# Optimization experiments

Hardware: AMD Instinct MI355X
Metric: run time of the kernel (lower is better)

The kernel has to match this reference:

```python
import jax, jax.numpy as jnp
import numpy as np

B, CIN, COUT, HIN = 2, 64, 64, 96
ALPHA = 0.2       # LeakyReLU slope in GAT
K_RANK = 6        # dist.argsort(1).argsort(1) <= 6  -> 7 nearest neighbors incl. self
DN = ('NCHW', 'OIHW', 'NCHW')


def setup_inputs():
    key = jax.random.key(0)
    ks = jax.random.split(key, 10)
    sc = lambda k, shape, s: jax.random.normal(k, shape, jnp.float32) * s
    return {
        'x': jax.random.normal(ks[0], (B, CIN, HIN, HIN), jnp.float32),
        'conv_w': sc(ks[1], (COUT, CIN, 3, 3), 0.05),
        'conv_b': jnp.zeros((COUT,), jnp.float32),
        'W1': sc(ks[2], (COUT, COUT), 0.1),
        'a1': sc(ks[3], (2 * COUT,), 0.1),
        'W2': sc(ks[4], (COUT, COUT), 0.1),
        'a2': sc(ks[5], (2 * COUT,), 0.1),
        'Wout': sc(ks[6], (2 * COUT, COUT), 0.1),
        'aout': sc(ks[7], (2 * COUT,), 0.1),
        'tconv_w': sc(ks[8], (COUT, COUT, 3, 3), 0.05),  # torch ConvTranspose2d layout [in,out,kh,kw]
        'tconv_b': jnp.zeros((COUT,), jnp.float32),
    }


def _gat_layer(h, adj, W, a, concat):
    # h: [B,N,F_in], W: [F_in,F_out], a: [2*F_out]
    Wh = h @ W                                   # [B,N,F']
    Fo = W.shape[1]
    e = (Wh @ a[:Fo])[:, :, None] + (Wh @ a[Fo:])[:, None, :]   # [B,N,N]
    e = jax.nn.leaky_relu(e, ALPHA)
    e = jnp.where(adj > 0, e, -9e15)
    attn = jax.nn.softmax(e, axis=-1)
    out = jnp.einsum('bij,bjf->bif', attn, Wh)
    return jax.nn.elu(out) if concat else out


def reference(x, conv_w, conv_b, W1, a1, W2, a2, Wout, aout, tconv_w, tconv_b):
    # --- Pre_ProcessLayer_Graph: stride-2 conv, flatten, 7-NN dense adjacency ---
    y = jax.lax.conv_general_dilated(x, conv_w, (2, 2), ((1, 1), (1, 1)),
                                     dimension_numbers=DN) + conv_b[None, :, None, None]
    Bb, C, H, W_ = y.shape
    N = H * W_
    feat = y.reshape(Bb, C, N).transpose(0, 2, 1)          # [B,N,C]
    sq = jnp.sum(feat * feat, axis=-1)                     # [B,N]
    d2 = sq[:, :, None] + sq[:, None, :] - 2.0 * jnp.einsum('bic,bjc->bij', feat, feat)
    dist = jnp.sqrt(jnp.maximum(d2, 0.0))                  # euclidean cdist
    ranks = jnp.argsort(jnp.argsort(dist, axis=-1), axis=-1)
    adj = (ranks <= K_RANK).astype(feat.dtype)             # [B,N,N] binary, incl. self (rank 0)
    # --- GAT (pyGAT style): 2 concat heads + output attention layer, eval mode ---
    h1 = _gat_layer(feat, adj, W1, a1, True)
    h2 = _gat_layer(feat, adj, W2, a2, True)
    hcat = jnp.concatenate([h1, h2], axis=-1)              # [B,N,2C]
    g = jax.nn.elu(_gat_layer(hcat, adj, Wout, aout, False))  # [B,N,C]
    # --- reshape back + transpose conv (k=3, s=2, p=1, output_padding=1) ---
    g = g.transpose(0, 2, 1).reshape(Bb, C, H, W_)
    wt = jnp.flip(tconv_w, (2, 3)).transpose(1, 0, 2, 3)   # -> [out,in,kh,kw]
    out = jax.lax.conv_general_dilated(g, wt, (1, 1), ((1, 2), (1, 2)),
                                       lhs_dilation=(2, 2),
                                       dimension_numbers=DN) + tconv_b[None, :, None, None]
    return out
```

## Files before the change

kernel.cpp:

```cpp
#include <hip/hip_runtime.h>
#include <hip/hip_bf16.h>
#include <stdint.h>

using bf16 = __hip_bfloat16;
using u64 = unsigned long long;

constexpr int B_ = 2;
constexpr int N_ = 2304;

constexpr int OFF_WC2   = 0;
constexpr int OFF_WT2   = 36864;
constexpr int OFF_W1F   = 73728;
constexpr int OFF_W2F   = 77824;
constexpr int OFF_WOUTF = 81920;
constexpr int OFF_A1F   = 90112;
constexpr int OFF_A2F   = 90240;
constexpr int OFF_AOUTF = 90368;
constexpr int OFF_CBF   = 90496;
constexpr int OFF_TBF   = 90560;
constexpr int OFF_FLAG  = 90624;
constexpr int OFF_SQ    = 90688;
constexpr int OFF_S11   = 95296;
constexpr int OFF_S12   = 99904;
constexpr int OFF_S21   = 104512;
constexpr int OFF_S22   = 109120;
constexpr int OFF_S1O   = 113728;
constexpr int OFF_S2O   = 118336;
constexpr int OFF_KNN   = 122944;
constexpr int OFF_BUF0  = 159808;
constexpr int OFF_BUF1  = 454720;
constexpr int OFF_BUF2  = 749632;
constexpr int OFF_BUF3  = 1044544;
constexpr int OFF_PK    = 1339456;

__device__ __forceinline__ float bf2f_raw(unsigned short u) {
    return __uint_as_float(((unsigned int)u) << 16);
}

__device__ __forceinline__ unsigned int mono32(float f) {
    unsigned int u = __float_as_uint(f);
    return (u & 0x80000000u) ? ~u : (u | 0x80000000u);
}

__device__ __forceinline__ bool detect_f32(const void* conv_w) {
    const unsigned short* cw = (const unsigned short*)conv_w;
    float m = 0.f;
    #pragma unroll
    for (int u = 0; u < 64; ++u) {
        float v = fabsf(bf2f_raw(cw[u]));
        if (v < 3.0e38f) m = fmaxf(m, v);
    }
    return m > 1.0e4f;
}

__global__ __launch_bounds__(256) void kc_prep(
    const void* conv_w, const void* conv_b, const void* W1, const void* a1,
    const void* W2, const void* a2, const void* Wout, const void* aout,
    const void* tconv_w, const void* tconv_b, float* __restrict__ ws)
{
    bool f32 = detect_f32(conv_w);
    int idx = blockIdx.x * 256 + threadIdx.x;
    if (idx == 0) ws[OFF_FLAG] = f32 ? 1.f : 0.f;
    if (idx < 32256) ws[OFF_SQ + idx] = 0.f;

    {
        int tap = idx >> 12, ic = (idx >> 6) & 63, oc = idx & 63;
        if (f32) {
            ws[OFF_WC2 + idx] = ((const float*)conv_w)[(oc * 64 + ic) * 9 + tap];
            ws[OFF_WT2 + idx] = ((const float*)tconv_w)[(ic * 64 + oc) * 9 + tap];
        } else {
            ws[OFF_WC2 + idx] = bf2f_raw(((const unsigned short*)conv_w)[(oc * 64 + ic) * 9 + tap]);
            ws[OFF_WT2 + idx] = bf2f_raw(((const unsigned short*)tconv_w)[(ic * 64 + oc) * 9 + tap]);
        }
    }
    if (idx < 4096) {
        if (f32) {
            ws[OFF_W1F + idx] = ((const float*)W1)[idx];
            ws[OFF_W2F + idx] = ((const float*)W2)[idx];
        } else {
            ws[OFF_W1F + idx] = bf2f_raw(((const unsigned short*)W1)[idx]);
            ws[OFF_W2F + idx] = bf2f_raw(((const unsigned short*)W2)[idx]);
        }
    }
    if (idx < 8192)
        ws[OFF_WOUTF + idx] = f32 ? ((const float*)Wout)[idx]
                                  : bf2f_raw(((const unsigned short*)Wout)[idx]);
    if (idx < 128) {
        if (f32) {
            ws[OFF_A1F + idx]   = ((const float*)a1)[idx];
            ws[OFF_A2F + idx]   = ((const float*)a2)[idx];
            ws[OFF_AOUTF + idx] = ((const float*)aout)[idx];
        } else {
            ws[OFF_A1F + idx]   = bf2f_raw(((const unsigned short*)a1)[idx]);
            ws[OFF_A2F + idx]   = bf2f_raw(((const unsigned short*)a2)[idx]);
            ws[OFF_AOUTF + idx] = bf2f_raw(((const unsigned short*)aout)[idx]);
        }
    }
    if (idx < 64) {
        if (f32) {
            ws[OFF_CBF + idx] = ((const float*)conv_b)[idx];
            ws[OFF_TBF + idx] = ((const float*)tconv_b)[idx];
        } else {
            ws[OFF_CBF + idx] = bf2f_raw(((const unsigned short*)conv_b)[idx]);
            ws[OFF_TBF + idx] = bf2f_raw(((const unsigned short*)tconv_b)[idx]);
        }
    }
}

template <bool F32>
__device__ __forceinline__ void conv_body(const void* __restrict__ x,
                                          float* __restrict__ ws,
                                          int n, int ocb, int b)
{
    int oy = n / 48, ox = n - (n / 48) * 48;
    const float* wc2 = ws + OFF_WC2;
    size_t xb = (size_t)b * 64 * 9216;
    float acc[4] = {0, 0, 0, 0};

    for (int ky = 0; ky < 3; ++ky) {
        int iy = 2 * oy - 1 + ky;
        bool vy = (unsigned)iy < 96u;
        int iyc = vy ? iy : 0;
        for (int kx = 0; kx < 3; ++kx) {
            int ix = 2 * ox - 1 + kx;
            bool v = vy && ((unsigned)ix < 96u);
            int ixc = v ? ix : 0;
            size_t xoff = xb + iyc * 96 + ixc;
            const float* wb = wc2 + (ky * 3 + kx) * 4096 + ocb;
            #pragma unroll 8
            for (int ic = 0; ic < 64; ++ic) {
                float xv;
                if (F32) xv = ((const float*)x)[xoff + ic * 9216];
                else     xv = bf2f_raw(((const unsigned short*)x)[xoff + ic * 9216]);
                xv = v ? xv : 0.f;
                const float* wr = wb + ic * 64;
                #pragma unroll
                for (int o = 0; o < 4; ++o) acc[o] += xv * wr[o];
            }
        }
    }
    float* featT = ws + OFF_BUF0 + (size_t)b * 64 * N_;
    const float* cb = ws + OFF_CBF;
    float ssum = 0.f;
    #pragma unroll
    for (int o = 0; o < 4; ++o) {
        float f = acc[o] + cb[ocb + o];
        acc[o] = f;
        featT[(ocb + o) * N_ + n] = f;
        ssum += f * f;
    }
    *(float4*)(ws + OFF_BUF2 + ((size_t)(b * N_ + n) * 64 + ocb)) =
        make_float4(acc[0], acc[1], acc[2], acc[3]);
    atomicAdd(ws + OFF_SQ + b * N_ + n, ssum);
}

__global__ __launch_bounds__(128) void k1_conv(const void* __restrict__ x,
                                               float* __restrict__ ws)
{
    int n   = blockIdx.x * 128 + threadIdx.x;
    int ocb = blockIdx.y * 4;
    int b   = blockIdx.z;
    if (ws[OFF_FLAG] != 0.f) conv_body<true >(x, ws, n, ocb, b);
    else                     conv_body<false>(x, ws, n, ocb, b);
}

__global__ __launch_bounds__(256) void k2_knn(float* __restrict__ ws)
{
    __shared__ float Bs[32][256];
    float* ysp = &Bs[0][0];
    int tid = threadIdx.x;
    int i0  = blockIdx.x * 16;
    int jh  = blockIdx.y;
    int b   = i0 / N_;
    const float* fT  = ws + OFF_BUF0 + (size_t)b * 64 * N_;
    const float* fnc = ws + OFF_BUF2;
    const float* sq  = ws + OFF_SQ + b * N_;
    int w = tid >> 6, lane = tid & 63;
    int r0 = w * 4;
    int arow0 = __builtin_amdgcn_readfirstlane(i0 + r0);

    u64 K[7];
    #pragma unroll
    for (int t = 0; t < 7; ++t) K[t] = ~0ull;

    int rsel = tid >> 4;
    int g    = tid & 15;

    for (int jt = 0; jt < 3; ++jt) {
        int jb = jh * 768 + jt * 256;
        float acc[4][4];
        #pragma unroll
        for (int r = 0; r < 4; ++r)
            #pragma unroll
            for (int c = 0; c < 4; ++c) acc[r][c] = 0.f;

        for (int kh = 0; kh < 2; ++kh) {
            __syncthreads();
            #pragma unroll
            for (int it = 0; it < 8; ++it) {
                int idx = tid + it * 256;
                int k = idx >> 6, j4 = idx & 63;
                float4 v = *(const float4*)(fT + (size_t)(kh * 32 + k) * N_ + jb + j4 * 4);
                *(float4*)&Bs[k][j4 * 4] = v;
            }
            __syncthreads();

            #pragma unroll 2
            for (int k4 = 0; k4 < 8; ++k4) {
                float4 Bv[4];
                #pragma unroll
                for (int kk = 0; kk < 4; ++kk)
                    Bv[kk] = *(const float4*)&Bs[k4 * 4 + kk][4 * lane];
                #pragma unroll
                for (int r = 0; r < 4; ++r) {
                    float4 a = *(const float4*)(fnc + (size_t)(arow0 + r) * 64
                                                + kh * 32 + k4 * 4);
                    acc[r][0] += a.x * Bv[0].x + a.y * Bv[1].x + a.z * Bv[2].x + a.w * Bv[3].x;
                    acc[r][1] += a.x * Bv[0].y + a.y * Bv[1].y + a.z * Bv[2].y + a.w * Bv[3].y;
                    acc[r][2] += a.x * Bv[0].z + a.y * Bv[1].z + a.z * Bv[2].z + a.w * Bv[3].z;
                    acc[r][3] += a.x * Bv[0].w + a.y * Bv[1].w + a.z * Bv[2].w + a.w * Bv[3].w;
                }
            }
        }

        __syncthreads();
        float4 sqv = *(const float4*)(sq + jb + 4 * lane);
        #pragma unroll
        for (int r = 0; r < 4; ++r) {
            float4 yv;
            yv.x = sqv.x - 2.f * acc[r][0];
            yv.y = sqv.y - 2.f * acc[r][1];
            yv.z = sqv.z - 2.f * acc[r][2];
            yv.w = sqv.w - 2.f * acc[r][3];
            *(float4*)&ysp[(r0 + r) * 264 + 4 * lane] = yv;
        }
        __syncthreads();

        #pragma unroll 4
        for (int u = 0; u < 16; ++u) {
            int jl = g + 16 * u;
            float y = ysp[rsel * 264 + jl];
            u64 key = ((u64)mono32(y) << 32) | (unsigned int)(jb + jl);
            if (key < K[6]) {
                int pos = 0;
                #pragma unroll
                for (int s = 0; s < 7; ++s) pos += (K[s] < key) ? 1 : 0;
                #pragma unroll
                for (int p = 6; p > 0; --p)
                    K[p] = (p == pos) ? key : ((p > pos) ? K[p - 1] : K[p]);
                if (pos == 0) K[0] = key;
            }
        }
        __syncthreads();
    }

    u64 myk = 0;
    for (int pass = 0; pass < 7; ++pass) {
        u64 m = K[0];
        #pragma unroll
        for (int s = 1; s < 7; ++s) m = (K[s] < m) ? K[s] : m;
        #pragma unroll
        for (int off = 1; off < 16; off <<= 1) {
            u64 o = (u64)__shfl_xor((long long)m, off);
            m = (o < m) ? o : m;
        }
        #pragma unroll
        for (int s = 0; s < 7; ++s)
            if (K[s] == m) K[s] = ~0ull;
        if (g == pass) myk = m;
    }
    if (g < 7) {
        u64* pk = (u64*)(ws + OFF_PK);
        pk[((size_t)(i0 + rsel) * 3 + jh) * 8 + g] = myk;
    }
}

__global__ __launch_bounds__(256) void k_lin(float* __restrict__ ws)
{
    int g = blockIdx.y;
    if (g == 32) {
        int row = blockIdx.x * 256 + threadIdx.x;
        const u64* pk = (const u64*)(ws + OFF_PK) + (size_t)row * 24;
        int* kout = (int*)(ws + OFF_KNN) + (size_t)row * 8;
        u64 L0[7], L1[7], L2[7];
        #pragma unroll
        for (int q = 0; q < 7; ++q) { L0[q] = pk[q]; L1[q] = pk[8 + q]; L2[q] = pk[16 + q]; }
        #pragma unroll
        for (int q = 0; q < 7; ++q) {
            int rank = q;
            #pragma unroll
            for (int p = 0; p < 7; ++p)
                rank += ((L1[p] < L0[q]) ? 1 : 0) + ((L2[p] < L0[q]) ? 1 : 0);
            if (rank < 7) kout[rank] = (int)(L0[q] & 0xffffffffull);
        }
        #pragma unroll
        for (int q = 0; q < 7; ++q) {
            int rank = q;
            #pragma unroll
            for (int p = 0; p < 7; ++p)
                rank += ((L0[p] < L1[q]) ? 1 : 0) + ((L2[p] < L1[q]) ? 1 : 0);
            if (rank < 7) kout[rank] = (int)(L1[q] & 0xffffffffull);
        }
        #pragma unroll
        for (int q = 0; q < 7; ++q) {
            int rank = q;
            #pragma unroll
            for (int p = 0; p < 7; ++p)
                rank += ((L0[p] < L2[q]) ? 1 : 0) + ((L1[p] < L2[q]) ? 1 : 0);
            if (rank < 7) kout[rank] = (int)(L2[q] & 0xffffffffull);
        }
        return;
    }
    int layer = g >> 4;
    int ocb = (g & 15) * 4;
    const float* W  = ws + (layer ? OFF_W2F : OFF_W1F);
    const float* a  = ws + (layer ? OFF_A2F : OFF_A1F);
    float* out_nc   = ws + (layer ? OFF_BUF3 : OFF_BUF1);
    float* s1       = ws + (layer ? OFF_S21 : OFF_S11);
    float* s2       = ws + (layer ? OFF_S22 : OFF_S12);
    int i = blockIdx.x * 256 + threadIdx.x;
    int b = i / N_, n = i - b * N_;
    const float* in_b = ws + OFF_BUF0 + (size_t)b * 64 * N_;

    float acc[4] = {0, 0, 0, 0};
    #pragma unroll 8
    for (int kk = 0; kk < 64; ++kk) {
        float xv = in_b[kk * N_ + n];
        const float* wr = W + kk * 64 + ocb;
        #pragma unroll
        for (int o = 0; o < 4; ++o) acc[o] += xv * wr[o];
    }
    *(float4*)(out_nc + ((size_t)i * 64 + ocb)) =
        make_float4(acc[0], acc[1], acc[2], acc[3]);
    float p1 = 0.f, p2 = 0.f;
    #pragma unroll
    for (int o = 0; o < 4; ++o) {
        p1 += acc[o] * a[ocb + o];
        p2 += acc[o] * a[64 + ocb + o];
    }
    atomicAdd(s1 + i, p1);
    atomicAdd(s2 + i, p2);
}

__global__ __launch_bounds__(256) void k_lin2(float* __restrict__ ws)
{
    int ocb = blockIdx.y * 4;
    int i = blockIdx.x * 256 + threadIdx.x;
    int b = i / N_, n = i - b * N_;
    const float* h1 = ws + OFF_BUF2 + (size_t)b * 64 * N_;
    const float* h2 = ws + OFF_BUF0 + (size_t)b * 64 * N_;
    const float* W  = ws + OFF_WOUTF;
    const float* a  = ws + OFF_AOUTF;

    float acc[4] = {0, 0, 0, 0};
    #pragma unroll 8
    for (int kk = 0; kk < 64; ++kk) {
        float xv = h1[kk * N_ + n];
        const float* wr = W + kk * 64 + ocb;
        #pragma unroll
        for (int o = 0; o < 4; ++o) acc[o] += xv * wr[o];
    }
    #pragma unroll 8
    for (int kk = 0; kk < 64; ++kk) {
        float xv = h2[kk * N_ + n];
        const float* wr = W + (64 + kk) * 64 + ocb;
        #pragma unroll
        for (int o = 0; o < 4; ++o) acc[o] += xv * wr[o];
    }
    *(float4*)(ws + OFF_BUF1 + ((size_t)i * 64 + ocb)) =
        make_float4(acc[0], acc[1], acc[2], acc[3]);
    float p1 = 0.f, p2 = 0.f;
    #pragma unroll
    for (int o = 0; o < 4; ++o) {
        p1 += acc[o] * a[ocb + o];
        p2 += acc[o] * a[64 + ocb + o];
    }
    atomicAdd(ws + OFF_S1O + i, p1);
    atomicAdd(ws + OFF_S2O + i, p2);
}

__device__ __forceinline__ void attn_body(
    const float* __restrict__ Wh_nc, const float* __restrict__ s1,
    const float* __restrict__ s2, const int* __restrict__ knn,
    float* __restrict__ out, int i, int b, int n, int c4)
{
    const int* kp = knn + (size_t)i * 8;
    int j[7];
    #pragma unroll
    for (int t = 0; t < 7; ++t) {
        int jt = kp[t];
        j[t] = ((unsigned)jt < (unsigned)N_) ? jt : 0;
    }
    float si = s1[i];
    const float* s2b = s2 + b * N_;
    float e[7];
    #pragma unroll
    for (int t = 0; t < 7; ++t) {
        float v = si + s2b[j[t]];
        e[t] = v > 0.f ? v : 0.2f * v;
    }
    float m = e[0];
    #pragma unroll
    for (int t = 1; t < 7; ++t) m = fmaxf(m, e[t]);
    float ssum = 0.f;
    #pragma unroll
    for (int t = 0; t < 7; ++t) { e[t] = __expf(e[t] - m); ssum += e[t]; }
    float inv = 1.f / ssum;
    #pragma unroll
    for (int t = 0; t < 7; ++t) e[t] *= inv;

    const float4* W4 = (const float4*)Wh_nc;
    float4 acc = make_float4(0.f, 0.f, 0.f, 0.f);
    #pragma unroll
    for (int t = 0; t < 7; ++t) {
        float4 v = W4[(size_t)(b * N_ + j[t]) * 16 + c4];
        acc.x += e[t] * v.x; acc.y += e[t] * v.y;
        acc.z += e[t] * v.z; acc.w += e[t] * v.w;
    }
    acc.x = acc.x > 0.f ? acc.x : expm1f(acc.x);
    acc.y = acc.y > 0.f ? acc.y : expm1f(acc.y);
    acc.z = acc.z > 0.f ? acc.z : expm1f(acc.z);
    acc.w = acc.w > 0.f ? acc.w : expm1f(acc.w);
    float* ob = out + (size_t)b * 64 * N_;
    ob[(c4 * 4 + 0) * N_ + n] = acc.x;
    ob[(c4 * 4 + 1) * N_ + n] = acc.y;
    ob[(c4 * 4 + 2) * N_ + n] = acc.z;
    ob[(c4 * 4 + 3) * N_ + n] = acc.w;
}

__global__ __launch_bounds__(256) void k_attn12(float* __restrict__ ws)
{
    int layer = blockIdx.z;
    const float* Wh_nc = ws + (layer ? OFF_BUF3 : OFF_BUF1);
    const float* s1    = ws + (layer ? OFF_S21 : OFF_S11);
    const float* s2    = ws + (layer ? OFF_S22 : OFF_S12);
    float* out         = ws + (layer ? OFF_BUF0 : OFF_BUF2);
    int c4 = blockIdx.y;
    int i = blockIdx.x * 256 + threadIdx.x;
    int b = i / N_, n = i - b * N_;
    attn_body(Wh_nc, s1, s2, (const int*)(ws + OFF_KNN), out, i, b, n, c4);
}

__global__ __launch_bounds__(256) void k_attn_out(float* __restrict__ ws)
{
    int c4 = blockIdx.y;
    int i = blockIdx.x * 256 + threadIdx.x;
    int b = i / N_, n = i - b * N_;
    attn_body(ws + OFF_BUF1, ws + OFF_S1O, ws + OFF_S2O,
              (const int*)(ws + OFF_KNN), ws + OFF_BUF3, i, b, n, c4);
}

__global__ __launch_bounds__(128) void k7_tconv(float* __restrict__ ws,
                                                void* __restrict__ outp)
{
    bool f32 = ws[OFF_FLAG] != 0.f;
    int pixc = blockIdx.x * 128 + threadIdx.x;
    int g    = blockIdx.y;
    int pc   = g >> 3, ocb = (g & 7) * 8;
    int b    = blockIdx.z;
    int py = pc >> 1, px = pc & 1;
    int ay = pixc / 48, bx = pixc - (pixc / 48) * 48;
    int oy = 2 * ay + py, ox = 2 * bx + px;

    const float* gT  = ws + OFF_BUF3 + (size_t)b * 64 * N_;
    const float* wt2 = ws + OFF_WT2;
    float acc[8] = {0, 0, 0, 0, 0, 0, 0, 0};

    int nky = py ? 2 : 1;
    int nkx = px ? 2 : 1;
    for (int s = 0; s < nky; ++s) {
        int ky = py ? (s == 0 ? 0 : 2) : 1;
        int iy = py ? (s == 0 ? ay + 1 : ay) : ay;
        bool vy = iy < 48;
        for (int t = 0; t < nkx; ++t) {
            int kx = px ? (t == 0 ? 0 : 2) : 1;
            int ix = px ? (t == 0 ? bx + 1 : bx) : bx;
            bool v = vy && (ix < 48);
            const float* gp = gT + (v ? iy * 48 + ix : 0);
            const float* wb = wt2 + (ky * 3 + kx) * 4096 + ocb;
            #pragma unroll 8
            for (int ic = 0; ic < 64; ++ic) {
                float gv = gp[ic * N_];
                gv = v ? gv : 0.f;
                const float* wr = wb + ic * 64;
                #pragma unroll
                for (int o = 0; o < 8; ++o) acc[o] += gv * wr[o];
            }
        }
    }
    const float* tb = ws + OFF_TBF;
    size_t base = ((size_t)(b * 64 + ocb) * 96 + oy) * 96 + ox;
    if (f32) {
        float* op = (float*)outp;
        #pragma unroll
        for (int o = 0; o < 8; ++o) op[base + (size_t)o * 9216] = acc[o] + tb[ocb + o];
    } else {
        bf16* op = (bf16*)outp;
        #pragma unroll
        for (int o = 0; o < 8; ++o)
            op[base + (size_t)o * 9216] = __float2bfloat16(acc[o] + tb[ocb + o]);
    }
}

extern "C" void kernel_launch(void* const* d_in, const int* in_sizes, int n_in,
                              void* d_out, int out_size, void* d_ws, size_t ws_size,
                              hipStream_t stream)
{
    float* ws = (float*)d_ws;

    hipLaunchKernelGGL(kc_prep, dim3(144), dim3(256), 0, stream,
                       d_in[1], d_in[2], d_in[3], d_in[4], d_in[5], d_in[6],
                       d_in[7], d_in[8], d_in[9], d_in[10], ws);
    hipLaunchKernelGGL(k1_conv, dim3(18, 16, 2), dim3(128), 0, stream, d_in[0], ws);
    hipLaunchKernelGGL(k2_knn, dim3(288, 3), dim3(256), 0, stream, ws);
    hipLaunchKernelGGL(k_lin, dim3(18, 33), dim3(256), 0, stream, ws);
    hipLaunchKernelGGL(k_attn12, dim3(18, 16, 2), dim3(256), 0, stream, ws);
    hipLaunchKernelGGL(k_lin2, dim3(18, 16), dim3(256), 0, stream, ws);
    hipLaunchKernelGGL(k_attn_out, dim3(18, 16), dim3(256), 0, stream, ws);
    hipLaunchKernelGGL(k7_tconv, dim3(18, 32, 2), dim3(128), 0, stream, ws, d_out);
}
```

Measured before the change: 230.7 us.

## Load kNN distance B-operand directly into registers with double-buffered prefetch

The kNN distance GEMM no longer stages the feature columns through shared memory. Each thread now loads its own float4 columns straight from global memory into two register buffers and prefetches the next k-slice while computing on the current one. Shared memory is cut down to a per-wave scratch for the distance rows, and every __syncthreads is dropped because each wave only reads the rows it wrote itself. The cost is that the four waves of a block each re-read the same columns from global memory and rely on cache hits, and register pressure rises.

```diff
diff --git a/kernel.cpp b/kernel.cpp
--- a/kernel.cpp
+++ b/kernel.cpp
@@ -166,8 +166,7 @@
 
 __global__ __launch_bounds__(256) void k2_knn(float* __restrict__ ws)
 {
-    __shared__ float Bs[32][256];
-    float* ysp = &Bs[0][0];
+    __shared__ float ys[16][264];
     int tid = threadIdx.x;
     int i0  = blockIdx.x * 16;
     int jh  = blockIdx.y;
@@ -186,44 +185,47 @@
     int rsel = tid >> 4;
     int g    = tid & 15;
 
+#define LOADB(dst, K4) do {                                                   \
+        const float* _p = colp + (size_t)(K4) * 4 * N_;                       \
+        dst[0] = *(const float4*)(_p);                                        \
+        dst[1] = *(const float4*)(_p + N_);                                   \
+        dst[2] = *(const float4*)(_p + 2 * N_);                               \
+        dst[3] = *(const float4*)(_p + 3 * N_);                               \
+    } while (0)
+
+#define FMAB(src, K4) do {                                                    \
+        _Pragma("unroll")                                                     \
+        for (int r = 0; r < 4; ++r) {                                         \
+                            \
+            float4 a = *(const float4*)(fnc + (size_t)(arow0 + r) * 64        \
+                                        + (K4) * 4);                          \
+            acc[r][0] += a.x*src[0].x + a.y*src[1].x + a.z*src[2].x + a.w*src[3].x; \
+            acc[r][1] += a.x*src[0].y + a.y*src[1].y + a.z*src[2].y + a.w*src[3].y; \
+            acc[r][2] += a.x*src[0].z + a.y*src[1].z + a.z*src[2].z + a.w*src[3].z; \
+            acc[r][3] += a.x*src[0].w + a.y*src[1].w + a.z*src[2].w + a.w*src[3].w; \
+        }                                                                     \
+    } while (0)
+
     for (int jt = 0; jt < 3; ++jt) {
         int jb = jh * 768 + jt * 256;
+        const float* colp = fT + jb + 4 * lane;
         float acc[4][4];
         #pragma unroll
         for (int r = 0; r < 4; ++r)
             #pragma unroll
             for (int c = 0; c < 4; ++c) acc[r][c] = 0.f;
 
-        for (int kh = 0; kh < 2; ++kh) {
-            __syncthreads();
-            #pragma unroll
-            for (int it = 0; it < 8; ++it) {
-                int idx = tid + it * 256;
-                int k = idx >> 6, j4 = idx & 63;
-                float4 v = *(const float4*)(fT + (size_t)(kh * 32 + k) * N_ + jb + j4 * 4);
-                *(float4*)&Bs[k][j4 * 4] = v;
-            }
-            __syncthreads();
-
-            #pragma unroll 2
-            for (int k4 = 0; k4 < 8; ++k4) {
-                float4 Bv[4];
-                #pragma unroll
-                for (int kk = 0; kk < 4; ++kk)
-                    Bv[kk] = *(const float4*)&Bs[k4 * 4 + kk][4 * lane];
-                #pragma unroll
-                for (int r = 0; r < 4; ++r) {
-                    float4 a = *(const float4*)(fnc + (size_t)(arow0 + r) * 64
-                                                + kh * 32 + k4 * 4);
-                    acc[r][0] += a.x * Bv[0].x + a.y * Bv[1].x + a.z * Bv[2].x + a.w * Bv[3].x;
-                    acc[r][1] += a.x * Bv[0].y + a.y * Bv[1].y + a.z * Bv[2].y + a.w * Bv[3].y;
-                    acc[r][2] += a.x * Bv[0].z + a.y * Bv[1].z + a.z * Bv[2].z + a.w * Bv[3].z;
-                    acc[r][3] += a.x * Bv[0].w + a.y * Bv[1].w + a.z * Bv[2].w + a.w * Bv[3].w;
-                }
-            }
-        }
-
-        __syncthreads();
+        float4 pA[4], pB[4];
+        LOADB(pA, 0);
+        LOADB(pB, 1);
+        #pragma unroll
+        for (int k4 = 0; k4 < 16; k4 += 2) {
+            FMAB(pA, k4);
+            if (k4 + 2 < 16) LOADB(pA, k4 + 2);
+            FMAB(pB, k4 + 1);
+            if (k4 + 3 < 16) LOADB(pB, k4 + 3);
+        }
+
         float4 sqv = *(const float4*)(sq + jb + 4 * lane);
         #pragma unroll
         for (int r = 0; r < 4; ++r) {
@@ -232,14 +234,13 @@
             yv.y = sqv.y - 2.f * acc[r][1];
             yv.z = sqv.z - 2.f * acc[r][2];
             yv.w = sqv.w - 2.f * acc[r][3];
-            *(float4*)&ysp[(r0 + r) * 264 + 4 * lane] = yv;
-        }
-        __syncthreads();
+            *(float4*)&ys[r0 + r][4 * lane] = yv;
+        }
 
         #pragma unroll 4
         for (int u = 0; u < 16; ++u) {
             int jl = g + 16 * u;
-            float y = ysp[rsel * 264 + jl];
+            float y = ys[rsel][jl];
             u64 key = ((u64)mono32(y) << 32) | (unsigned int)(jb + jl);
             if (key < K[6]) {
                 int pos = 0;
@@ -251,8 +252,9 @@
                 if (pos == 0) K[0] = key;
             }
         }
-        __syncthreads();
-    }
+    }
+#undef LOADB
+#undef FMAB
 
     u64 myk = 0;
     for (int pass = 0; pass < 7; ++pass) {
```

Measured after the change: 258.8 us. +12.2%, slower.

## Double-buffer kNN distance tiles with async global-to-LDS loads

Applied to the files above, without the earlier changes.

The k2_knn distance GEMM now splits the K dimension into four 16-wide slices. Each slice is staged into a double-buffered shared tile with global_load_lds, so the next slice loads while the current one is computed. The next tile's first slice is prefetched during the top-k selection, and the distance scratch gets its own buffer, which removes a barrier because each wave reads only rows it wrote itself. This cuts barrier count and register-staged copies, at the cost of more shared memory and reliance on the barrier waiting for the async LDS writes.

```diff
diff --git a/kernel.cpp b/kernel.cpp
--- a/kernel.cpp
+++ b/kernel.cpp
@@ -166,8 +166,8 @@
 
 __global__ __launch_bounds__(256) void k2_knn(float* __restrict__ ws)
 {
-    __shared__ float Bs[32][256];
-    float* ysp = &Bs[0][0];
+    __shared__ float Bs[2][16][256];
+    __shared__ float ys[16][260];
     int tid = threadIdx.x;
     int i0  = blockIdx.x * 16;
     int jh  = blockIdx.y;
@@ -186,6 +186,23 @@
     int rsel = tid >> 4;
     int g    = tid & 15;
 
+#define STAGE(BI, JB, KQ) do {                                                \
+        _Pragma("unroll")                                                     \
+        for (int it_ = 0; it_ < 4; ++it_) {                                   \
+            int idx_ = tid + it_ * 256;                                       \
+            int k_ = idx_ >> 6, j4_ = idx_ & 63;                              \
+            __builtin_amdgcn_global_load_lds(                                 \
+                (const __attribute__((address_space(1))) unsigned int*)       \
+                    (fT + (size_t)((KQ) * 16 + k_) * N_ + (JB) + j4_ * 4),    \
+                (__attribute__((address_space(3))) unsigned int*)             \
+                    &Bs[BI][k_][j4_ * 4],                                     \
+                16, 0, 0);                                                    \
+        }                                                                     \
+    } while (0)
+
+    STAGE(0, jh * 768, 0);
+    __syncthreads();
+
     for (int jt = 0; jt < 3; ++jt) {
         int jb = jh * 768 + jt * 256;
         float acc[4][4];
@@ -194,36 +211,34 @@
             #pragma unroll
             for (int c = 0; c < 4; ++c) acc[r][c] = 0.f;
 
-        for (int kh = 0; kh < 2; ++kh) {
-            __syncthreads();
+        #pragma unroll
+        for (int kq = 0; kq < 4; ++kq) {
+            if (kq < 3) STAGE((kq + 1) & 1, jb, kq + 1);
+
             #pragma unroll
-            for (int it = 0; it < 8; ++it) {
-                int idx = tid + it * 256;
-                int k = idx >> 6, j4 = idx & 63;
-                float4 v = *(const float4*)(fT + (size_t)(kh * 32 + k) * N_ + jb + j4 * 4);
-                *(float4*)&Bs[k][j4 * 4] = v;
-            }
-            __syncthreads();
-
-            #pragma unroll 2
-            for (int k4 = 0; k4 < 8; ++k4) {
+            for (int k4 = 0; k4 < 4; ++k4) {
                 float4 Bv[4];
                 #pragma unroll
                 for (int kk = 0; kk < 4; ++kk)
-                    Bv[kk] = *(const float4*)&Bs[k4 * 4 + kk][4 * lane];
+                    Bv[kk] = *(const float4*)&Bs[kq & 1][k4 * 4 + kk][4 * lane];
                 #pragma unroll
                 for (int r = 0; r < 4; ++r) {
                     float4 a = *(const float4*)(fnc + (size_t)(arow0 + r) * 64
-                                                + kh * 32 + k4 * 4);
+                                                + kq * 16 + k4 * 4);
                     acc[r][0] += a.x * Bv[0].x + a.y * Bv[1].x + a.z * Bv[2].x + a.w * Bv[3].x;
                     acc[r][1] += a.x * Bv[0].y + a.y * Bv[1].y + a.z * Bv[2].y + a.w * Bv[3].y;
                     acc[r][2] += a.x * Bv[0].z + a.y * Bv[1].z + a.z * Bv[2].z + a.w * Bv[3].z;
                     acc[r][3] += a.x * Bv[0].w + a.y * Bv[1].w + a.z * Bv[2].w + a.w * Bv[3].w;
                 }
             }
-        }
-
-        __syncthreads();
+
+            if (kq < 3) {
+                __syncthreads();
+            }
+        }
+
+        if (jt < 2) STAGE(0, jb + 256, 0);
+
         float4 sqv = *(const float4*)(sq + jb + 4 * lane);
         #pragma unroll
         for (int r = 0; r < 4; ++r) {
@@ -232,14 +247,13 @@
             yv.y = sqv.y - 2.f * acc[r][1];
             yv.z = sqv.z - 2.f * acc[r][2];
             yv.w = sqv.w - 2.f * acc[r][3];
-            *(float4*)&ysp[(r0 + r) * 264 + 4 * lane] = yv;
-        }
-        __syncthreads();
+            *(float4*)&ys[r0 + r][4 * lane] = yv;
+        }
 
         #pragma unroll 4
         for (int u = 0; u < 16; ++u) {
             int jl = g + 16 * u;
-            float y = ysp[rsel * 264 + jl];
+            float y = ys[rsel][jl];
             u64 key = ((u64)mono32(y) << 32) | (unsigned int)(jb + jl);
             if (key < K[6]) {
                 int pos = 0;
@@ -251,8 +265,10 @@
                 if (pos == 0) K[0] = key;
             }
         }
-        __syncthreads();
-    }
+
+        if (jt < 2) __syncthreads();
+    }
+#undef STAGE
 
     u64 myk = 0;
     for (int pass = 0; pass < 7; ++pass) {
```

Measured after the change: 351.4 us. 52.3% more time.
